# Optimization experiments

Hardware: AMD Instinct MI355X
Metric: run time of the kernel (lower is better)

## Reference

```python
import jax, jax.numpy as jnp
import numpy as np

E = 768
H = 12
D = E // H  # head_dim = 64
EPS = 1e-6
SCALE = D ** -0.5


def _l2norm(x, eps=EPS):
    # torch F.normalize: x / clamp_min(||x||_2, eps)
    n = jnp.sqrt(jnp.sum(x * x, axis=-1, keepdims=True))
    return x / jnp.maximum(n, eps)


def setup_inputs() -> dict:
    key = jax.random.key(0)
    ks = jax.random.split(key, 12)
    B, S = 2, 2048
    w = lambda k: jax.random.normal(k, (E, E), dtype=jnp.float32) * 0.02
    b = lambda k: jax.random.normal(k, (E,), dtype=jnp.float32) * 0.02
    return {
        "query": jax.random.normal(ks[0], (B, S, E), dtype=jnp.float32),
        "key": jax.random.normal(ks[1], (B, S, E), dtype=jnp.float32),
        "value": jax.random.normal(ks[2], (B, S, E), dtype=jnp.float32),
        "Wq": w(ks[3]), "bq": b(ks[4]),
        "Wk": w(ks[5]), "bk": b(ks[6]),
        "Wv": w(ks[7]), "bv": b(ks[8]),
        "Wo": w(ks[9]), "bo": b(ks[10]),
    }


def reference(query, key, value, Wq, bq, Wk, bk, Wv, bv, Wo, bo):
    B, T, _ = query.shape
    S = key.shape[1]
    # nn.Linear: x @ W.T + b; then split heads -> [B, H, S, D]
    split = lambda x, L: x.reshape(B, L, H, D).transpose(0, 2, 1, 3)
    q = split(query @ Wq.T + bq, T)
    k = split(key @ Wk.T + bk, S)
    v = split(value @ Wv.T + bv, S)
    q = _l2norm(q)
    k = _l2norm(k)
    scores = jnp.einsum("bhtd,bhsd->bhts", q, k) * SCALE
    attn = jax.nn.softmax(scores, axis=-1)
    ctx = jnp.einsum("bhts,bhsd->bhtd", attn, v)
    ctx = ctx.transpose(0, 2, 1, 3).reshape(B, T, E)
    return ctx @ Wo.T + bo
```

## Files before the change

### kernel.cpp

```cpp
#include <hip/hip_runtime.h>
#include <hip/hip_bf16.h>

#define EE 768
#define HH 12
#define DD 64
#define BB 2
#define SS 2048
#define MM (BB*SS)
#define NT (MM*EE)
#define NW (EE*EE)

typedef short short8 __attribute__((ext_vector_type(8)));
typedef float f32x4 __attribute__((ext_vector_type(4)));

static __device__ __forceinline__ unsigned short f2bf(float f) {
    unsigned int u = __float_as_uint(f);
    u += 0x7fffu + ((u >> 16) & 1u);
    return (unsigned short)(u >> 16);
}

static __device__ __forceinline__ void gl16(const void* g, void* l) {
    __builtin_amdgcn_global_load_lds(
        (const __attribute__((address_space(1))) unsigned int*)g,
        (__attribute__((address_space(3))) unsigned int*)l, 16, 0, 0);
}

static __device__ __forceinline__ int swz(int row, int chunk) {
    return row * 128 + ((chunk ^ (row & 7)) << 4);
}

__global__ __launch_bounds__(256) void cvt_all_kernel(
    const float* __restrict__ xq, const float* __restrict__ xk, const float* __restrict__ xv,
    const float* __restrict__ wq, const float* __restrict__ wk,
    const float* __restrict__ wv, const float* __restrict__ wo,
    unsigned short* __restrict__ oq, unsigned short* __restrict__ ok, unsigned short* __restrict__ ov,
    unsigned short* __restrict__ owq, unsigned short* __restrict__ owk,
    unsigned short* __restrict__ owv, unsigned short* __restrict__ owo)
{
    const int XQ = NT / 4;
    const int WQ = NW / 4;
    const int idx = blockIdx.x * 256 + threadIdx.x;
    const float* s;
    unsigned short* d;
    int off;
    if (idx < 3 * XQ) {
        const int r = idx / XQ;
        off = idx - r * XQ;
        s = (r == 0) ? xq : (r == 1) ? xk : xv;
        d = (r == 0) ? oq : (r == 1) ? ok : ov;
    } else {
        const int j = idx - 3 * XQ;
        const int r = j / WQ;
        off = j - r * WQ;
        s = (r == 0) ? wq : (r == 1) ? wk : (r == 2) ? wv : wo;
        d = (r == 0) ? owq : (r == 1) ? owk : (r == 2) ? owv : owo;
    }
    float4 f = ((const float4*)s)[off];
    ushort4 u;
    u.x = f2bf(f.x); u.y = f2bf(f.y); u.z = f2bf(f.z); u.w = f2bf(f.w);
    ((ushort4*)d)[off] = u;
}

__global__ __launch_bounds__(256) void qkv_mfma_kernel(
    const unsigned short* __restrict__ xq, const unsigned short* __restrict__ xk,
    const unsigned short* __restrict__ xv,
    const unsigned short* __restrict__ Wq, const float* __restrict__ bq,
    const unsigned short* __restrict__ Wk, const float* __restrict__ bk,
    const unsigned short* __restrict__ Wv, const float* __restrict__ bv,
    unsigned short* __restrict__ qo, unsigned short* __restrict__ ko,
    unsigned short* __restrict__ vo)
{
    __shared__ short As[128 * 64];
    __shared__ short Bs[64 * 64];
    __shared__ float ssq[2][128];

    const int tid = threadIdx.x;
    const int bm  = blockIdx.x * 128;
    const int by  = blockIdx.y;
    const int proj = by / 12;
    const int h    = by % 12;
    const int n0r  = h * 64;

    const unsigned short* x = (proj == 0) ? xq : (proj == 1) ? xk : xv;
    const unsigned short* W = (proj == 0) ? Wq : (proj == 1) ? Wk : Wv;
    const float* bias       = (proj == 0) ? bq : (proj == 1) ? bk : bv;

    const int w  = tid >> 6;
    const int l  = tid & 63;
    const int c  = l & 15;
    const int g  = l >> 4;
    const int wm = w >> 1;
    const int wn = w & 1;
    const int lr8 = l >> 3;
    const int lc8 = (l & 7) ^ lr8;

    f32x4 acc[4][2] = {};

    for (int kt = 0; kt < EE; kt += 64) {
        __syncthreads();
        #pragma unroll
        for (int i = 0; i < 4; ++i) {
            const int t = w * 4 + i;
            gl16(x + (size_t)(bm + t * 8 + lr8) * EE + kt + lc8 * 8,
                 (unsigned short*)As + t * 512);
        }
        #pragma unroll
        for (int i = 0; i < 2; ++i) {
            const int t = w * 2 + i;
            gl16(W + (size_t)(n0r + t * 8 + lr8) * EE + kt + lc8 * 8,
                 (unsigned short*)Bs + t * 512);
        }
        __syncthreads();

        #pragma unroll
        for (int ks = 0; ks < 2; ++ks) {
            short8 bfr[2], afr[4];
            #pragma unroll
            for (int nt = 0; nt < 2; ++nt)
                bfr[nt] = *(const short8*)((const char*)Bs + swz(wn * 32 + nt * 16 + c, ks * 4 + g));
            #pragma unroll
            for (int mt = 0; mt < 4; ++mt)
                afr[mt] = *(const short8*)((const char*)As + swz(wm * 64 + mt * 16 + c, ks * 4 + g));
            #pragma unroll
            for (int mt = 0; mt < 4; ++mt)
                #pragma unroll
                for (int nt = 0; nt < 2; ++nt)
                    acc[mt][nt] = __builtin_amdgcn_mfma_f32_16x16x32_bf16(
                        afr[mt], bfr[nt], acc[mt][nt], 0, 0, 0);
        }
    }
    __syncthreads();

    float bb[2];
    #pragma unroll
    for (int nt = 0; nt < 2; ++nt) bb[nt] = bias[n0r + wn * 32 + nt * 16 + c];

    const int bidx  = bm >> 11;
    const int sbase = bm & (SS - 1);

    if (proj < 2) {
        f32x4 vr[4][2];
        f32x4 ssp[4];
        #pragma unroll
        for (int mt = 0; mt < 4; ++mt) {
            #pragma unroll
            for (int nt = 0; nt < 2; ++nt)
                #pragma unroll
                for (int j = 0; j < 4; ++j)
                    vr[mt][nt][j] = acc[mt][nt][j] + bb[nt];
            #pragma unroll
            for (int j = 0; j < 4; ++j)
                ssp[mt][j] = vr[mt][0][j]*vr[mt][0][j] + vr[mt][1][j]*vr[mt][1][j];
            #pragma unroll
            for (int j = 0; j < 4; ++j) {
                float s = ssp[mt][j];
                #pragma unroll
                for (int msk = 1; msk < 16; msk <<= 1) s += __shfl_xor(s, msk);
                ssp[mt][j] = s;
            }
        }
        if (c == 0) {
            #pragma unroll
            for (int mt = 0; mt < 4; ++mt)
                #pragma unroll
                for (int j = 0; j < 4; ++j)
                    ssq[wn][wm * 64 + mt * 16 + g * 4 + j] = ssp[mt][j];
        }
        __syncthreads();
        unsigned short* dst = (proj == 0) ? qo : ko;
        const float fold = (proj == 0) ? 0.18033688f : 1.0f;
        #pragma unroll
        for (int mt = 0; mt < 4; ++mt) {
            #pragma unroll
            for (int j = 0; j < 4; ++j) {
                const int rloc = wm * 64 + mt * 16 + g * 4 + j;
                const float ss = ssq[0][rloc] + ssq[1][rloc];
                const float inv = fold / fmaxf(sqrtf(ss), 1e-6f);
                const size_t base =
                    ((size_t)(bidx * HH + h) * SS + sbase + rloc) * DD;
                #pragma unroll
                for (int nt = 0; nt < 2; ++nt)
                    dst[base + wn * 32 + nt * 16 + c] = f2bf(vr[mt][nt][j] * inv);
            }
        }
    } else {
        #pragma unroll
        for (int mt = 0; mt < 4; ++mt)
            #pragma unroll
            for (int nt = 0; nt < 2; ++nt)
                #pragma unroll
                for (int j = 0; j < 4; ++j) {
                    const int row = wm * 64 + mt * 16 + g * 4 + j;
                    const int col = wn * 32 + nt * 16 + c;
                    As[row * 64 + col] = (short)f2bf(acc[mt][nt][j] + bb[nt]);
                }
        __syncthreads();
        const int d  = tid & 63;
        const int sb = (tid >> 6) * 32;
        unsigned short* dstp = vo + ((size_t)(bidx * HH + h) * DD + d) * SS + sbase + sb;
        #pragma unroll
        for (int grp = 0; grp < 4; ++grp) {
            unsigned int wds[4];
            #pragma unroll
            for (int e = 0; e < 4; ++e) {
                unsigned short u0 = (unsigned short)As[(sb + grp * 8 + 2 * e)     * 64 + d];
                unsigned short u1 = (unsigned short)As[(sb + grp * 8 + 2 * e + 1) * 64 + d];
                wds[e] = (unsigned int)u0 | ((unsigned int)u1 << 16);
            }
            int4 pk = make_int4((int)wds[0], (int)wds[1], (int)wds[2], (int)wds[3]);
            *(int4*)(dstp + grp * 8) = pk;
        }
    }
}

static __device__ __forceinline__ void stage_kv4(
    const unsigned short* __restrict__ kbase, const unsigned short* __restrict__ vbase,
    int s0, short* Kbuf, short* Vbuf, int w, int lr8, int lc8)
{
    #pragma unroll
    for (int i = 0; i < 2; ++i) {
        const int t = w * 2 + i;
        gl16(kbase + (size_t)(s0 + t * 8 + lr8) * DD + lc8 * 8,
             (unsigned short*)Kbuf + t * 512);
    }
    #pragma unroll
    for (int i = 0; i < 2; ++i) {
        const int t = w * 2 + i;
        gl16(vbase + (size_t)(t * 8 + lr8) * SS + s0 + lc8 * 8,
             (unsigned short*)Vbuf + t * 512);
    }
}

__global__ __launch_bounds__(256) void attn_mfma_kernel(
    const unsigned short* __restrict__ q, const unsigned short* __restrict__ k,
    const unsigned short* __restrict__ vT, unsigned short* __restrict__ ctx)
{
    __shared__ short Ks[2][64 * 64];
    __shared__ short Vs[2][64 * 64];
    __shared__ short Ps[4][16 * 64];

    const int tid = threadIdx.x;
    const int bh  = blockIdx.y;
    const int w   = tid >> 6;
    const int l   = tid & 63;
    const int c   = l & 15;
    const int g   = l >> 4;
    const int lr8 = l >> 3;
    const int lc8 = (l & 7) ^ lr8;
    const int qr0 = blockIdx.x * 64 + w * 16;

    const unsigned short* kbase = k  + (size_t)bh * SS * DD;
    const unsigned short* vbase = vT + (size_t)bh * DD * SS;

    short8 aq[2];
    {
        const unsigned short* qg = q + ((size_t)bh * SS + qr0 + c) * DD;
        aq[0] = *(const short8*)(qg + g * 8);
        aq[1] = *(const short8*)(qg + 32 + g * 8);
    }
    const short one_bf = (short)0x3F80;
    short8 ones = {one_bf, one_bf, one_bf, one_bf, one_bf, one_bf, one_bf, one_bf};

    short* Psw = Ps[w];
    f32x4 o[4] = {};
    f32x4 lacc = {0.f, 0.f, 0.f, 0.f};

    stage_kv4(kbase, vbase, 0, Ks[0], Vs[0], w, lr8, lc8);
    __syncthreads();

    for (int t = 0; t < SS / 64; ++t) {
        const int cur = t & 1;
        if (t + 1 < SS / 64)
            stage_kv4(kbase, vbase, (t + 1) * 64, Ks[cur ^ 1], Vs[cur ^ 1], w, lr8, lc8);

        f32x4 sc[4] = {};
        #pragma unroll
        for (int ks = 0; ks < 2; ++ks)
            #pragma unroll
            for (int nt = 0; nt < 4; ++nt) {
                short8 kf = *(const short8*)((const char*)Ks[cur] + swz(nt * 16 + c, ks * 4 + g));
                sc[nt] = __builtin_amdgcn_mfma_f32_16x16x32_bf16(aq[ks], kf, sc[nt], 0, 0, 0);
            }

        #pragma unroll
        for (int nt = 0; nt < 4; ++nt)
            #pragma unroll
            for (int j = 0; j < 4; ++j) {
                const float p = __builtin_exp2f(sc[nt][j]);
                const int row = g * 4 + j;
                const int ch  = (nt * 2 + (c >> 3)) ^ (row & 7);
                Psw[row * 64 + (ch << 3) + (c & 7)] = (short)f2bf(p);
            }

        #pragma unroll
        for (int ks = 0; ks < 2; ++ks) {
            short8 pa = *(const short8*)((const char*)Psw + swz(c, ks * 4 + g));
            lacc = __builtin_amdgcn_mfma_f32_16x16x32_bf16(pa, ones, lacc, 0, 0, 0);
            #pragma unroll
            for (int dt = 0; dt < 4; ++dt) {
                short8 vf = *(const short8*)((const char*)Vs[cur] + swz(dt * 16 + c, ks * 4 + g));
                o[dt] = __builtin_amdgcn_mfma_f32_16x16x32_bf16(pa, vf, o[dt], 0, 0, 0);
            }
        }
        __syncthreads();
    }

    const int bidx = bh / HH, h = bh % HH;
    #pragma unroll
    for (int j = 0; j < 4; ++j) {
        const float inv = 1.0f / lacc[j];
        const int sg = qr0 + g * 4 + j;
        unsigned short* op = ctx + ((size_t)bidx * SS + sg) * EE + h * DD + c;
        #pragma unroll
        for (int dt = 0; dt < 4; ++dt)
            op[dt * 16] = f2bf(o[dt][j] * inv);
    }
}

__global__ __launch_bounds__(256) void out_mfma_kernel(
    const unsigned short* __restrict__ A, const unsigned short* __restrict__ W,
    const float* __restrict__ bias, float* __restrict__ out)
{
    __shared__ short As[128 * 64];
    __shared__ short Bs[64 * 64];

    const int tid = threadIdx.x;
    const int bm  = blockIdx.x * 128;
    const int n0  = blockIdx.y * 64;

    const int w  = tid >> 6;
    const int l  = tid & 63;
    const int c  = l & 15;
    const int g  = l >> 4;
    const int wm = w >> 1;
    const int wn = w & 1;
    const int lr8 = l >> 3;
    const int lc8 = (l & 7) ^ lr8;

    f32x4 acc[4][2] = {};

    for (int kt = 0; kt < EE; kt += 64) {
        __syncthreads();
        #pragma unroll
        for (int i = 0; i < 4; ++i) {
            const int t = w * 4 + i;
            gl16(A + (size_t)(bm + t * 8 + lr8) * EE + kt + lc8 * 8,
                 (unsigned short*)As + t * 512);
        }
        #pragma unroll
        for (int i = 0; i < 2; ++i) {
            const int t = w * 2 + i;
            gl16(W + (size_t)(n0 + t * 8 + lr8) * EE + kt + lc8 * 8,
                 (unsigned short*)Bs + t * 512);
        }
        __syncthreads();

        #pragma unroll
        for (int ks = 0; ks < 2; ++ks) {
            short8 bfr[2], afr[4];
            #pragma unroll
            for (int nt = 0; nt < 2; ++nt)
                bfr[nt] = *(const short8*)((const char*)Bs + swz(wn * 32 + nt * 16 + c, ks * 4 + g));
            #pragma unroll
            for (int mt = 0; mt < 4; ++mt)
                afr[mt] = *(const short8*)((const char*)As + swz(wm * 64 + mt * 16 + c, ks * 4 + g));
            #pragma unroll
            for (int mt = 0; mt < 4; ++mt)
                #pragma unroll
                for (int nt = 0; nt < 2; ++nt)
                    acc[mt][nt] = __builtin_amdgcn_mfma_f32_16x16x32_bf16(
                        afr[mt], bfr[nt], acc[mt][nt], 0, 0, 0);
        }
    }

    float bb[2];
    #pragma unroll
    for (int nt = 0; nt < 2; ++nt) bb[nt] = bias[n0 + wn * 32 + nt * 16 + c];

    #pragma unroll
    for (int mt = 0; mt < 4; ++mt)
        #pragma unroll
        for (int j = 0; j < 4; ++j) {
            const int row = bm + wm * 64 + mt * 16 + g * 4 + j;
            float* op = out + (size_t)row * EE + n0 + wn * 32 + c;
            #pragma unroll
            for (int nt = 0; nt < 2; ++nt)
                op[nt * 16] = acc[mt][nt][j] + bb[nt];
        }
}

extern "C" void kernel_launch(void* const* d_in, const int* in_sizes, int n_in,
                              void* d_out, int out_size, void* d_ws, size_t ws_size,
                              hipStream_t stream)
{
    const float* query = (const float*)d_in[0];
    const float* key   = (const float*)d_in[1];
    const float* value = (const float*)d_in[2];
    const float* Wq = (const float*)d_in[3];
    const float* bq = (const float*)d_in[4];
    const float* Wk = (const float*)d_in[5];
    const float* bk = (const float*)d_in[6];
    const float* Wv = (const float*)d_in[7];
    const float* bv = (const float*)d_in[8];
    const float* Wo = (const float*)d_in[9];
    const float* bo = (const float*)d_in[10];
    float* out = (float*)d_out;

    unsigned short* xqc  = (unsigned short*)d_ws;
    unsigned short* xkc  = xqc  + NT;
    unsigned short* xvc  = xkc  + NT;
    unsigned short* qws  = xvc  + NT;
    unsigned short* kws  = qws  + NT;
    unsigned short* vtws = kws  + NT;
    unsigned short* wqc  = vtws + NT;
    unsigned short* wkc  = wqc  + NW;
    unsigned short* wvc  = wkc  + NW;
    unsigned short* woc  = wvc  + NW;
    unsigned short* ctx  = xqc;

    const int cvt_blocks = (3 * (NT / 4) + 4 * (NW / 4)) / 256;
    cvt_all_kernel<<<dim3(cvt_blocks), 256, 0, stream>>>(
        query, key, value, Wq, Wk, Wv, Wo,
        xqc, xkc, xvc, wqc, wkc, wvc, woc);
    qkv_mfma_kernel<<<dim3(MM / 128, 36), 256, 0, stream>>>(
        xqc, xkc, xvc, wqc, bq, wkc, bk, wvc, bv, qws, kws, vtws);
    attn_mfma_kernel<<<dim3(SS / 64, BB * HH), 256, 0, stream>>>(
        qws, kws, vtws, ctx);
    out_mfma_kernel<<<dim3(MM / 128, EE / 64), 256, 0, stream>>>(
        ctx, woc, bo, out);
}
```

Before: 202.5 us.

## Widen QKV projection tile to two heads per block, drop cross-wave norm sync

The QKV projection block now computes a 128x128 output tile (two heads) instead of 128x64, so each A tile loaded from global memory is reused across twice as many columns and the grid halves. Because each wave column now owns a whole head, the L2 row norm is reduced entirely within the wave by shuffles, removing the shared-memory partial-sum array and its barrier. The cost is more accumulator registers per thread (16 f32x4), which may lower occupancy, plus a larger shared-memory tile for the V transpose.

```diff
diff --git a/kernel.cpp b/kernel.cpp
--- a/kernel.cpp
+++ b/kernel.cpp
@@ -70,16 +70,16 @@
     unsigned short* __restrict__ qo, unsigned short* __restrict__ ko,
     unsigned short* __restrict__ vo)
 {
-    __shared__ short As[128 * 64];
-    __shared__ short Bs[64 * 64];
-    __shared__ float ssq[2][128];
+    __shared__ short SMEM[128 * 128];
+    short* As = SMEM;
+    short* Bs = SMEM + 128 * 64;
 
     const int tid = threadIdx.x;
     const int bm  = blockIdx.x * 128;
     const int by  = blockIdx.y;
-    const int proj = by / 12;
-    const int h    = by % 12;
-    const int n0r  = h * 64;
+    const int proj = by / 6;
+    const int hp   = by % 6;
+    const int n0r  = hp * 128;
 
     const unsigned short* x = (proj == 0) ? xq : (proj == 1) ? xk : xv;
     const unsigned short* W = (proj == 0) ? Wq : (proj == 1) ? Wk : Wv;
@@ -94,7 +94,7 @@
     const int lr8 = l >> 3;
     const int lc8 = (l & 7) ^ lr8;
 
-    f32x4 acc[4][2] = {};
+    f32x4 acc[4][4] = {};
 
     for (int kt = 0; kt < EE; kt += 64) {
         __syncthreads();
@@ -105,8 +105,8 @@
                  (unsigned short*)As + t * 512);
         }
         #pragma unroll
-        for (int i = 0; i < 2; ++i) {
-            const int t = w * 2 + i;
+        for (int i = 0; i < 4; ++i) {
+            const int t = w * 4 + i;
             gl16(W + (size_t)(n0r + t * 8 + lr8) * EE + kt + lc8 * 8,
                  (unsigned short*)Bs + t * 512);
         }
@@ -114,97 +114,81 @@
 
         #pragma unroll
         for (int ks = 0; ks < 2; ++ks) {
-            short8 bfr[2], afr[4];
-            #pragma unroll
-            for (int nt = 0; nt < 2; ++nt)
-                bfr[nt] = *(const short8*)((const char*)Bs + swz(wn * 32 + nt * 16 + c, ks * 4 + g));
+            short8 bfr[4], afr[4];
+            #pragma unroll
+            for (int nt = 0; nt < 4; ++nt)
+                bfr[nt] = *(const short8*)((const char*)Bs + swz(wn * 64 + nt * 16 + c, ks * 4 + g));
             #pragma unroll
             for (int mt = 0; mt < 4; ++mt)
                 afr[mt] = *(const short8*)((const char*)As + swz(wm * 64 + mt * 16 + c, ks * 4 + g));
             #pragma unroll
             for (int mt = 0; mt < 4; ++mt)
                 #pragma unroll
-                for (int nt = 0; nt < 2; ++nt)
+                for (int nt = 0; nt < 4; ++nt)
                     acc[mt][nt] = __builtin_amdgcn_mfma_f32_16x16x32_bf16(
                         afr[mt], bfr[nt], acc[mt][nt], 0, 0, 0);
         }
     }
     __syncthreads();
 
-    float bb[2];
-    #pragma unroll
-    for (int nt = 0; nt < 2; ++nt) bb[nt] = bias[n0r + wn * 32 + nt * 16 + c];
+    float bb[4];
+    #pragma unroll
+    for (int nt = 0; nt < 4; ++nt) bb[nt] = bias[n0r + wn * 64 + nt * 16 + c];
 
     const int bidx  = bm >> 11;
     const int sbase = bm & (SS - 1);
+    const int head  = hp * 2 + wn;
 
     if (proj < 2) {
-        f32x4 vr[4][2];
-        f32x4 ssp[4];
-        #pragma unroll
-        for (int mt = 0; mt < 4; ++mt) {
-            #pragma unroll
-            for (int nt = 0; nt < 2; ++nt)
-                #pragma unroll
-                for (int j = 0; j < 4; ++j)
-                    vr[mt][nt][j] = acc[mt][nt][j] + bb[nt];
-            #pragma unroll
-            for (int j = 0; j < 4; ++j)
-                ssp[mt][j] = vr[mt][0][j]*vr[mt][0][j] + vr[mt][1][j]*vr[mt][1][j];
-            #pragma unroll
-            for (int j = 0; j < 4; ++j) {
-                float s = ssp[mt][j];
-                #pragma unroll
-                for (int msk = 1; msk < 16; msk <<= 1) s += __shfl_xor(s, msk);
-                ssp[mt][j] = s;
-            }
-        }
-        if (c == 0) {
-            #pragma unroll
-            for (int mt = 0; mt < 4; ++mt)
-                #pragma unroll
-                for (int j = 0; j < 4; ++j)
-                    ssq[wn][wm * 64 + mt * 16 + g * 4 + j] = ssp[mt][j];
-        }
-        __syncthreads();
         unsigned short* dst = (proj == 0) ? qo : ko;
         const float fold = (proj == 0) ? 0.18033688f : 1.0f;
         #pragma unroll
         for (int mt = 0; mt < 4; ++mt) {
+            f32x4 vr[4];
+            #pragma unroll
+            for (int nt = 0; nt < 4; ++nt)
+                #pragma unroll
+                for (int j = 0; j < 4; ++j)
+                    vr[nt][j] = acc[mt][nt][j] + bb[nt];
             #pragma unroll
             for (int j = 0; j < 4; ++j) {
+                float s = vr[0][j]*vr[0][j] + vr[1][j]*vr[1][j]
+                        + vr[2][j]*vr[2][j] + vr[3][j]*vr[3][j];
+                #pragma unroll
+                for (int msk = 1; msk < 16; msk <<= 1) s += __shfl_xor(s, msk);
+                const float inv = fold / fmaxf(sqrtf(s), 1e-6f);
                 const int rloc = wm * 64 + mt * 16 + g * 4 + j;
-                const float ss = ssq[0][rloc] + ssq[1][rloc];
-                const float inv = fold / fmaxf(sqrtf(ss), 1e-6f);
                 const size_t base =
-                    ((size_t)(bidx * HH + h) * SS + sbase + rloc) * DD;
-                #pragma unroll
-                for (int nt = 0; nt < 2; ++nt)
-                    dst[base + wn * 32 + nt * 16 + c] = f2bf(vr[mt][nt][j] * inv);
+                    ((size_t)(bidx * HH + head) * SS + sbase + rloc) * DD;
+                #pragma unroll
+                for (int nt = 0; nt < 4; ++nt)
+                    dst[base + nt * 16 + c] = f2bf(vr[nt][j] * inv);
             }
         }
     } else {
         #pragma unroll
         for (int mt = 0; mt < 4; ++mt)
             #pragma unroll
-            for (int nt = 0; nt < 2; ++nt)
+            for (int nt = 0; nt < 4; ++nt)
                 #pragma unroll
                 for (int j = 0; j < 4; ++j) {
                     const int row = wm * 64 + mt * 16 + g * 4 + j;
-                    const int col = wn * 32 + nt * 16 + c;
-                    As[row * 64 + col] = (short)f2bf(acc[mt][nt][j] + bb[nt]);
+                    const int col = wn * 64 + nt * 16 + c;
+                    SMEM[row * 128 + col] = (short)f2bf(acc[mt][nt][j] + bb[nt]);
                 }
         __syncthreads();
-        const int d  = tid & 63;
-        const int sb = (tid >> 6) * 32;
-        unsigned short* dstp = vo + ((size_t)(bidx * HH + h) * DD + d) * SS + sbase + sb;
-        #pragma unroll
-        for (int grp = 0; grp < 4; ++grp) {
+        const int d   = tid & 127;
+        const int sb  = (tid >> 7) * 64;
+        const int hd  = hp * 2 + (d >> 6);
+        const int dd  = d & 63;
+        unsigned short* dstp = vo + ((size_t)(bidx * HH + hd) * DD + dd) * SS + sbase + sb;
+        #pragma unroll
+        for (int grp = 0; grp < 8; ++grp) {
             unsigned int wds[4];
             #pragma unroll
             for (int e = 0; e < 4; ++e) {
-                unsigned short u0 = (unsigned short)As[(sb + grp * 8 + 2 * e)     * 64 + d];
-                unsigned short u1 = (unsigned short)As[(sb + grp * 8 + 2 * e + 1) * 64 + d];
+                unsigned short u0 = (unsigned short)SMEM[(sb + grp * 8 + 2 * e)     * 128 + d];
+                unsigned short u1 = (unsigned short)SMEM[(sb + grp * 8 + 2 * e + 1) * 128 + d];
                 wds[e] = (unsigned int)u0 | ((unsigned int)u1 << 16);
             }
             int4 pk = make_int4((int)wds[0], (int)wds[1], (int)wds[2], (int)wds[3]);
@@ -422,7 +406,7 @@
     cvt_all_kernel<<<dim3(cvt_blocks), 256, 0, stream>>>(
         query, key, value, Wq, Wk, Wv, Wo,
         xqc, xkc, xvc, wqc, wkc, wvc, woc);
-    qkv_mfma_kernel<<<dim3(MM / 128, 36), 256, 0, stream>>>(
+    qkv_mfma_kernel<<<dim3(MM / 128, 18), 256, 0, stream>>>(
         xqc, xkc, xvc, wqc, bq, wkc, bk, wvc, bv, qws, kws, vtws);
     attn_mfma_kernel<<<dim3(SS / 64, BB * HH), 256, 0, stream>>>(
         qws, kws, vtws, ctx);
```

Result: slower. 210.6 us (+4.0%).
